# Performance work log

Hardware: AMD Instinct MI355X
Metric: run time of the kernel (lower is better)

Reference implementation:

```python
import jax, jax.numpy as jnp
import numpy as np

H = 4       # hidden size
IN = 906    # input size
B = 128
T = 512


def _lstm_dir(xp, W_hh):
    """Run a single-direction LSTM. xp: [B, T, 4H] precomputed input projection
    (x @ W_ih^T + b_ih + b_hh). Returns hidden states [B, T, H].
    Torch gate order: i, f, g, o."""
    Bb = xp.shape[0]
    h0 = jnp.zeros((Bb, H), xp.dtype)
    c0 = jnp.zeros((Bb, H), xp.dtype)

    def step(carry, g_t):
        h, c = carry
        g = g_t + h @ W_hh.T                      # [B, 4H]
        i, f, gg, o = jnp.split(g, 4, axis=-1)
        i = jax.nn.sigmoid(i)
        f = jax.nn.sigmoid(f)
        gg = jnp.tanh(gg)
        o = jax.nn.sigmoid(o)
        c = f * c + i * gg
        h = o * jnp.tanh(c)
        return (h, c), h

    xs = jnp.swapaxes(xp, 0, 1)                   # [T, B, 4H]
    _, hs = jax.lax.scan(step, (h0, c0), xs)      # hs: [T, B, H]
    return jnp.swapaxes(hs, 0, 1)                 # [B, T, H]


def setup_inputs() -> dict:
    key = jax.random.key(0)
    ks = jax.random.split(key, 12)
    s = 1.0 / np.sqrt(H)  # torch nn.LSTM init scale
    d = {
        "x": jax.random.normal(ks[0], (B, T, IN), jnp.float32),
        "W_ih_f": jax.random.normal(ks[1], (4 * H, IN), jnp.float32) * s,
        "W_hh_f": jax.random.normal(ks[2], (4 * H, H), jnp.float32) * s,
        "b_ih_f": jax.random.normal(ks[3], (4 * H,), jnp.float32) * s,
        "b_hh_f": jax.random.normal(ks[4], (4 * H,), jnp.float32) * s,
        "W_ih_b": jax.random.normal(ks[5], (4 * H, IN), jnp.float32) * s,
        "W_hh_b": jax.random.normal(ks[6], (4 * H, H), jnp.float32) * s,
        "b_ih_b": jax.random.normal(ks[7], (4 * H,), jnp.float32) * s,
        "b_hh_b": jax.random.normal(ks[8], (4 * H,), jnp.float32) * s,
        "W_out": jax.random.normal(ks[9], (2, 2 * H), jnp.float32) * s,
        "b_out": jax.random.normal(ks[10], (2,), jnp.float32) * s,
    }
    return d


def reference(x, W_ih_f, W_hh_f, b_ih_f, b_hh_f, W_ih_b, W_hh_b, b_ih_b, b_hh_b, W_out, b_out):
    # forward direction
    xp_f = x @ W_ih_f.T + (b_ih_f + b_hh_f)       # [B, T, 4H]
    out_f = _lstm_dir(xp_f, W_hh_f)               # [B, T, H]
    # backward direction: process reversed sequence, then flip back to align time
    xr = x[:, ::-1]
    xp_b = xr @ W_ih_b.T + (b_ih_b + b_hh_b)
    out_b = _lstm_dir(xp_b, W_hh_b)[:, ::-1]      # [B, T, H]
    # r_out[:, -1, :] = concat(fwd last step, bwd output at last time index)
    last = jnp.concatenate([out_f[:, -1], out_b[:, -1]], axis=-1)  # [B, 2H]
    return last @ W_out.T + b_out                 # [B, 2]
```

## Files before the change

### kernel.cpp

```cpp
#include <hip/hip_runtime.h>

#define IN 906
#define TT 512
#define NB 128

__device__ __forceinline__ float fsigm(float x) {
    float e = __builtin_amdgcn_exp2f(-1.4426950408889634f * x);
    return __builtin_amdgcn_rcpf(1.f + e);
}
__device__ __forceinline__ float ftanh(float x) {
    float e = __builtin_amdgcn_exp2f(-2.8853900817779268f * x);
    return 2.f * __builtin_amdgcn_rcpf(1.f + e) - 1.f;
}
template <int M>
__device__ __forceinline__ float quad_bcast(float v) {
    constexpr int ctrl = M | (M << 2) | (M << 4) | (M << 6);
    return __int_as_float(
        __builtin_amdgcn_mov_dpp(__float_as_int(v), ctrl, 0xf, 0xf, true));
}

__global__ __launch_bounds__(256)
void gemm_xp(const float* __restrict__ x, const float* __restrict__ W,
             const float* __restrict__ b1, const float* __restrict__ b2,
             float* __restrict__ xp)
{
    __shared__ float sx[2][32][132];
    __shared__ float sw[2][32][16];
    const int tid = threadIdx.x;
    const size_t rowbase = (size_t)blockIdx.x * 128;

    const int srow = tid >> 1;
    const int sseg = tid & 1;
    const float* __restrict__ xrow = x + (rowbase + srow) * IN + sseg * 16;
    const int wout = tid >> 4;
    const int wcc  = (tid & 15) * 2;

    const int rg = tid >> 2;
    const int og = tid & 3;
    const int r0 = rg * 2;

    float2 xr[8];
    float2 wr;
    float acc[2][4];
#pragma unroll
    for (int r = 0; r < 2; ++r)
#pragma unroll
        for (int m = 0; m < 4; ++m) acc[r][m] = 0.f;

    auto load_chunk = [&](int c) {
        const int k0 = c * 32;
        if (c < 28) {
#pragma unroll
            for (int q = 0; q < 8; ++q)
                xr[q] = *(const float2*)(xrow + k0 + q * 2);
            wr = *(const float2*)(W + wout * IN + k0 + wcc);
        } else {
#pragma unroll
            for (int q = 0; q < 8; ++q) {
                int col = k0 + sseg * 16 + q * 2;
                xr[q].x = (col     < IN) ? xrow[k0 + q * 2]     : 0.f;
                xr[q].y = (col + 1 < IN) ? xrow[k0 + q * 2 + 1] : 0.f;
            }
            int colw = k0 + wcc;
            wr.x = (colw     < IN) ? W[wout * IN + colw]     : 0.f;
            wr.y = (colw + 1 < IN) ? W[wout * IN + colw + 1] : 0.f;
        }
    };
    auto write_chunk = [&](int buf) {
#pragma unroll
        for (int q = 0; q < 8; ++q) {
            int cc = sseg * 16 + q * 2;
            sx[buf][cc][srow]     = xr[q].x;
            sx[buf][cc + 1][srow] = xr[q].y;
        }
        sw[buf][wcc][wout]     = wr.x;
        sw[buf][wcc + 1][wout] = wr.y;
    };
    auto compute = [&](int buf) {
#pragma unroll
        for (int cc = 0; cc < 32; ++cc) {
            float2 xv = *(const float2*)&sx[buf][cc][r0];
            float4 wv = *(const float4*)&sw[buf][cc][og * 4];
            acc[0][0] = fmaf(xv.x, wv.x, acc[0][0]);
            acc[0][1] = fmaf(xv.x, wv.y, acc[0][1]);
            acc[0][2] = fmaf(xv.x, wv.z, acc[0][2]);
            acc[0][3] = fmaf(xv.x, wv.w, acc[0][3]);
            acc[1][0] = fmaf(xv.y, wv.x, acc[1][0]);
            acc[1][1] = fmaf(xv.y, wv.y, acc[1][1]);
            acc[1][2] = fmaf(xv.y, wv.z, acc[1][2]);
            acc[1][3] = fmaf(xv.y, wv.w, acc[1][3]);
        }
    };

    load_chunk(0);
    write_chunk(0);
    __syncthreads();
    for (int c = 0; c < 29; ++c) {
        if (c < 28) load_chunk(c + 1);
        compute(c & 1);
        if (c < 28) write_chunk((c + 1) & 1);
        __syncthreads();
    }

#pragma unroll
    for (int rr = 0; rr < 2; ++rr) {
        const size_t row = rowbase + r0 + rr;
#pragma unroll
        for (int m = 0; m < 4; ++m) {
            int j = og * 4 + m;
            xp[row * 16 + m * 4 + og] = acc[rr][m] + b1[j] + b2[j];
        }
    }
}

__global__ __launch_bounds__(256)
void frec(const float* __restrict__ xp, const float* __restrict__ x,
          const float* __restrict__ Whh, const float* __restrict__ Wb,
          const float* __restrict__ bb1, const float* __restrict__ bb2,
          const float* __restrict__ Wout, const float* __restrict__ bout,
          float* __restrict__ out)
{
    __shared__ float bg[16][12];
    const int tid = threadIdx.x;

    float h0 = 0.f, h1 = 0.f, h2 = 0.f, h3 = 0.f;

    if (tid >= 64) {
        const int gl = tid - 64;
        const int r  = gl >> 4;
        const int bq = gl & 15;
        const int b  = blockIdx.x * 16 + bq;
        const int gr = (r < 4) ? r : r + 4;
        const float2* __restrict__ xr  = (const float2*)(x + ((size_t)b * TT + (TT - 1)) * IN);
        const float2* __restrict__ wrp = (const float2*)(Wb + gr * IN);
        float s0 = 0.f, s1 = 0.f;
        int j = 0;
        for (; j + 8 <= 453; j += 8) {
#pragma unroll
            for (int u = 0; u < 8; ++u) {
                float2 a = xr[j + u];
                float2 w = wrp[j + u];
                s0 = fmaf(a.x, w.x, s0);
                s1 = fmaf(a.y, w.y, s1);
            }
        }
        for (; j < 453; ++j) {
            float2 a = xr[j];
            float2 w = wrp[j];
            s0 = fmaf(a.x, w.x, s0);
            s1 = fmaf(a.y, w.y, s1);
        }
        bg[bq][r] = s0 + s1 + bb1[gr] + bb2[gr];
    } else {
        const int k = tid & 3;
        const int b = blockIdx.x * 16 + (tid >> 2);

        float Wi[4], Wf4[4], Wg[4], Wo[4];
#pragma unroll
        for (int m = 0; m < 4; ++m) {
            Wi[m]  = Whh[(k)      * 4 + m];
            Wf4[m] = Whh[(4 + k)  * 4 + m];
            Wg[m]  = Whh[(8 + k)  * 4 + m];
            Wo[m]  = Whh[(12 + k) * 4 + m];
        }

        const float4* __restrict__ xq = (const float4*)xp;
        const size_t base = (size_t)b * TT * 4 + k;

        float4 pf[16];
#pragma unroll
        for (int i = 0; i < 16; ++i) pf[i] = xq[base + (size_t)i * 4];

        float c = 0.f;
        for (int t = 0; t < TT; t += 16) {
#pragma unroll
            for (int u = 0; u < 16; ++u) {
                float4 cur = pf[u];
                int tn = t + 16 + u;
                int tc = (tn < TT) ? tn : (TT - 1);
                pf[u] = xq[base + (size_t)tc * 4];

                float gi = cur.x + h0 * Wi[0]  + h1 * Wi[1]  + h2 * Wi[2]  + h3 * Wi[3];
                float gf = cur.y + h0 * Wf4[0] + h1 * Wf4[1] + h2 * Wf4[2] + h3 * Wf4[3];
                float gg = cur.z + h0 * Wg[0]  + h1 * Wg[1]  + h2 * Wg[2]  + h3 * Wg[3];
                float go = cur.w + h0 * Wo[0]  + h1 * Wo[1]  + h2 * Wo[2]  + h3 * Wo[3];

                float si = fsigm(gi);
                float sf = fsigm(gf);
                float tg = ftanh(gg);
                float so = fsigm(go);

                c = sf * c + si * tg;
                float h = so * ftanh(c);

                h0 = quad_bcast<0>(h);
                h1 = quad_bcast<1>(h);
                h2 = quad_bcast<2>(h);
                h3 = quad_bcast<3>(h);
            }
        }
    }

    __syncthreads();

    if (tid < 64) {
        const int k  = tid & 3;
        const int bq = tid >> 2;
        const int b  = blockIdx.x * 16 + bq;

        float gib = bg[bq][k];
        float ggb = bg[bq][4 + k];
        float gob = bg[bq][8 + k];
        float hbk = fsigm(gob) * ftanh(fsigm(gib) * ftanh(ggb));
        float hb0 = quad_bcast<0>(hbk);
        float hb1 = quad_bcast<1>(hbk);
        float hb2 = quad_bcast<2>(hbk);
        float hb3 = quad_bcast<3>(hbk);

        float o0 = bout[0]
                 + h0  * Wout[0]  + h1  * Wout[1]  + h2  * Wout[2]  + h3  * Wout[3]
                 + hb0 * Wout[4]  + hb1 * Wout[5]  + hb2 * Wout[6]  + hb3 * Wout[7];
        float o1 = bout[1]
                 + h0  * Wout[8]  + h1  * Wout[9]  + h2  * Wout[10] + h3  * Wout[11]
                 + hb0 * Wout[12] + hb1 * Wout[13] + hb2 * Wout[14] + hb3 * Wout[15];

        if (k == 0) {
            out[b * 2 + 0] = o0;
            out[b * 2 + 1] = o1;
        }
    }
}

extern "C" void kernel_launch(void* const* d_in, const int* in_sizes, int n_in,
                              void* d_out, int out_size, void* d_ws, size_t ws_size,
                              hipStream_t stream)
{
    const float* x    = (const float*)d_in[0];
    const float* Wihf = (const float*)d_in[1];
    const float* Whhf = (const float*)d_in[2];
    const float* bihf = (const float*)d_in[3];
    const float* bhhf = (const float*)d_in[4];
    const float* Wihb = (const float*)d_in[5];
    const float* bihb = (const float*)d_in[7];
    const float* bhhb = (const float*)d_in[8];
    const float* Wout = (const float*)d_in[9];
    const float* bout = (const float*)d_in[10];

    float* xp = (float*)d_ws;

    gemm_xp<<<512, 256, 0, stream>>>(x, Wihf, bihf, bhhf, xp);
    frec<<<8, 256, 0, stream>>>(xp, x, Whhf, Wihb, bihb, bhhb, Wout, bout,
                                (float*)d_out);
}
```

Baseline: 434.9 us.

## Rewrite input-projection GEMM as split-K register accumulation with shuffle transpose-reduce

Replaces the LDS-tiled GEMM with a scheme where each wave handles 8 rows, every lane holds a k-slice, and all 8x16 outputs are accumulated in 128 registers. A recursive-halving butterfly of xor shuffles then reduces across the 64 lanes and scatters the results into xp. The shared-memory staging and per-chunk barriers go away, and x is read with coalesced float2 loads. In exchange register pressure is very high under the 2-waves-per-SIMD launch bound, the reduction adds shuffle overhead, and the grid grows to 2048 blocks.

After: 456.0 us. 1.05x slower.

```diff
diff --git a/kernel.cpp b/kernel.cpp
--- a/kernel.cpp
+++ b/kernel.cpp
@@ -19,98 +19,111 @@
         __builtin_amdgcn_mov_dpp(__float_as_int(v), ctrl, 0xf, 0xf, true));
 }
 
-__global__ __launch_bounds__(256)
+__global__ __launch_bounds__(256, 2)
 void gemm_xp(const float* __restrict__ x, const float* __restrict__ W,
              const float* __restrict__ b1, const float* __restrict__ b2,
              float* __restrict__ xp)
 {
-    __shared__ float sx[2][32][132];
-    __shared__ float sw[2][32][16];
     const int tid = threadIdx.x;
-    const size_t rowbase = (size_t)blockIdx.x * 128;
-
-    const int srow = tid >> 1;
-    const int sseg = tid & 1;
-    const float* __restrict__ xrow = x + (rowbase + srow) * IN + sseg * 16;
-    const int wout = tid >> 4;
-    const int wcc  = (tid & 15) * 2;
-
-    const int rg = tid >> 2;
-    const int og = tid & 3;
-    const int r0 = rg * 2;
-
-    float2 xr[8];
-    float2 wr;
-    float acc[2][4];
-#pragma unroll
-    for (int r = 0; r < 2; ++r)
-#pragma unroll
-        for (int m = 0; m < 4; ++m) acc[r][m] = 0.f;
-
-    auto load_chunk = [&](int c) {
-        const int k0 = c * 32;
-        if (c < 28) {
-#pragma unroll
-            for (int q = 0; q < 8; ++q)
-                xr[q] = *(const float2*)(xrow + k0 + q * 2);
-            wr = *(const float2*)(W + wout * IN + k0 + wcc);
+    const int l   = tid & 63;
+    const size_t row0 = (size_t)blockIdx.x * 32 + (size_t)(tid >> 6) * 8;
+
+    float acc[128];
+#pragma unroll
+    for (int i = 0; i < 128; ++i) acc[i] = 0.f;
+
+    const int kl = l * 2;
+
+#pragma unroll
+    for (int s = 0; s < 8; ++s) {
+        const int k = s * 128 + kl;
+        float2 wv[16];
+        float2 xv[8];
+        if (s < 7) {
+#pragma unroll
+            for (int jj = 0; jj < 16; ++jj)
+                wv[jj] = *(const float2*)(W + jj * IN + k);
+#pragma unroll
+            for (int r = 0; r < 8; ++r)
+                xv[r] = *(const float2*)(x + (row0 + r) * IN + k);
         } else {
-#pragma unroll
-            for (int q = 0; q < 8; ++q) {
-                int col = k0 + sseg * 16 + q * 2;
-                xr[q].x = (col     < IN) ? xrow[k0 + q * 2]     : 0.f;
-                xr[q].y = (col + 1 < IN) ? xrow[k0 + q * 2 + 1] : 0.f;
-            }
-            int colw = k0 + wcc;
-            wr.x = (colw     < IN) ? W[wout * IN + colw]     : 0.f;
-            wr.y = (colw + 1 < IN) ? W[wout * IN + colw + 1] : 0.f;
-        }
-    };
-    auto write_chunk = [&](int buf) {
-#pragma unroll
-        for (int q = 0; q < 8; ++q) {
-            int cc = sseg * 16 + q * 2;
-            sx[buf][cc][srow]     = xr[q].x;
-            sx[buf][cc + 1][srow] = xr[q].y;
-        }
-        sw[buf][wcc][wout]     = wr.x;
-        sw[buf][wcc + 1][wout] = wr.y;
-    };
-    auto compute = [&](int buf) {
-#pragma unroll
-        for (int cc = 0; cc < 32; ++cc) {
-            float2 xv = *(const float2*)&sx[buf][cc][r0];
-            float4 wv = *(const float4*)&sw[buf][cc][og * 4];
-            acc[0][0] = fmaf(xv.x, wv.x, acc[0][0]);
-            acc[0][1] = fmaf(xv.x, wv.y, acc[0][1]);
-            acc[0][2] = fmaf(xv.x, wv.z, acc[0][2]);
-            acc[0][3] = fmaf(xv.x, wv.w, acc[0][3]);
-            acc[1][0] = fmaf(xv.y, wv.x, acc[1][0]);
-            acc[1][1] = fmaf(xv.y, wv.y, acc[1][1]);
-            acc[1][2] = fmaf(xv.y, wv.z, acc[1][2]);
-            acc[1][3] = fmaf(xv.y, wv.w, acc[1][3]);
-        }
-    };
-
-    load_chunk(0);
-    write_chunk(0);
-    __syncthreads();
-    for (int c = 0; c < 29; ++c) {
-        if (c < 28) load_chunk(c + 1);
-        compute(c & 1);
-        if (c < 28) write_chunk((c + 1) & 1);
-        __syncthreads();
-    }
-
-#pragma unroll
-    for (int rr = 0; rr < 2; ++rr) {
-        const size_t row = rowbase + r0 + rr;
-#pragma unroll
-        for (int m = 0; m < 4; ++m) {
-            int j = og * 4 + m;
-            xp[row * 16 + m * 4 + og] = acc[rr][m] + b1[j] + b2[j];
-        }
-    }
+            const int  kc = (k < IN) ? k : 904;
+            const bool ok = (k < IN);
+#pragma unroll
+            for (int jj = 0; jj < 16; ++jj) {
+                float2 t = *(const float2*)(W + jj * IN + kc);
+                wv[jj].x = ok ? t.x : 0.f;
+                wv[jj].y = ok ? t.y : 0.f;
+            }
+#pragma unroll
+            for (int r = 0; r < 8; ++r)
+                xv[r] = *(const float2*)(x + (row0 + r) * IN + kc);
+        }
+#pragma unroll
+        for (int r = 0; r < 8; ++r)
+#pragma unroll
+            for (int jj = 0; jj < 16; ++jj) {
+                acc[r * 16 + jj] = fmaf(xv[r].x, wv[jj].x, acc[r * 16 + jj]);
+                acc[r * 16 + jj] = fmaf(xv[r].y, wv[jj].y, acc[r * 16 + jj]);
+            }
+    }
+
+    float v1[64];
+#pragma unroll
+    for (int i = 0; i < 64; ++i) {
+        float lo = acc[2 * i], hi = acc[2 * i + 1];
+        float mi = (l & 1) ? hi : lo;
+        float ot = (l & 1) ? lo : hi;
+        v1[i] = mi + __shfl_xor(ot, 1);
+    }
+    float v2[32];
+#pragma unroll
+    for (int i = 0; i < 32; ++i) {
+        float lo = v1[2 * i], hi = v1[2 * i + 1];
+        float mi = (l & 2) ? hi : lo;
+        float ot = (l & 2) ? lo : hi;
+        v2[i] = mi + __shfl_xor(ot, 2);
+    }
+    float v3[16];
+#pragma unroll
+    for (int i = 0; i < 16; ++i) {
+        float lo = v2[2 * i], hi = v2[2 * i + 1];
+        float mi = (l & 4) ? hi : lo;
+        float ot = (l & 4) ? lo : hi;
+        v3[i] = mi + __shfl_xor(ot, 4);
+    }
+    float v4[8];
+#pragma unroll
+    for (int i = 0; i < 8; ++i) {
+        float lo = v3[2 * i], hi = v3[2 * i + 1];
+        float mi = (l & 8) ? hi : lo;
+        float ot = (l & 8) ? lo : hi;
+        v4[i] = mi + __shfl_xor(ot, 8);
+    }
+    float v5[4];
+#pragma unroll
+    for (int i = 0; i < 4; ++i) {
+        float lo = v4[2 * i], hi = v4[2 * i + 1];
+        float mi = (l & 16) ? hi : lo;
+        float ot = (l & 16) ? lo : hi;
+        v5[i] = mi + __shfl_xor(ot, 16);
+    }
+    float v6[2];
+#pragma unroll
+    for (int i = 0; i < 2; ++i) {
+        float lo = v5[2 * i], hi = v5[2 * i + 1];
+        float mi = (l & 32) ? hi : lo;
+        float ot = (l & 32) ? lo : hi;
+        v6[i] = mi + __shfl_xor(ot, 32);
+    }
+
+    const int jo = l & 15;
+    const int g  = (l >> 4) & 3;
+    const int pj = (jo & 3) * 4 + (jo >> 2);
+    const float bias = b1[jo] + b2[jo];
+#pragma unroll
+    for (int p = 0; p < 2; ++p)
+        xp[(row0 + (size_t)(p * 4 + g)) * 16 + pj] = v6[p] + bias;
 }
 
 __global__ __launch_bounds__(256)
@@ -248,7 +261,7 @@
 
     float* xp = (float*)d_ws;
 
-    gemm_xp<<<512, 256, 0, stream>>>(x, Wihf, bihf, bhhf, xp);
+    gemm_xp<<<2048, 256, 0, stream>>>(x, Wihf, bihf, bhhf, xp);
     frec<<<8, 256, 0, stream>>>(xp, x, Whhf, Wihb, bihb, bhhb, Wout, bout,
                                 (float*)d_out);
 }
```

## Split GEMM K-chunk across two thread halves with 4x4 register tiles

Applied to the files above, without the earlier changes.

In the input-projection GEMM, each thread now computes a 4-row by 4-output register tile over half of each 32-wide K chunk instead of a 2x4 tile over the full chunk. The two thread halves split K and combine their partial sums through shared memory at the end. This improves the FMA-to-LDS-load ratio per thread with wider float4 row loads. It adds a final reduction pass with an extra barrier, leaves half the threads idle during the store phase, and raises per-thread register use.

Measured after the change: 433.1 us, median of 2. About the same (-0.4%).

```diff
diff --git a/kernel.cpp b/kernel.cpp
--- a/kernel.cpp
+++ b/kernel.cpp
@@ -35,15 +35,17 @@
     const int wout = tid >> 4;
     const int wcc  = (tid & 15) * 2;
 
-    const int rg = tid >> 2;
-    const int og = tid & 3;
-    const int r0 = rg * 2;
+    const int kh  = tid >> 7;
+    const int rem = tid & 127;
+    const int rg  = rem >> 2;
+    const int og  = rem & 3;
+    const int r0  = rg * 4;
 
     float2 xr[8];
     float2 wr;
-    float acc[2][4];
-#pragma unroll
-    for (int r = 0; r < 2; ++r)
+    float acc[4][4];
+#pragma unroll
+    for (int r = 0; r < 4; ++r)
 #pragma unroll
         for (int m = 0; m < 4; ++m) acc[r][m] = 0.f;
 
@@ -78,8 +80,9 @@
     };
     auto compute = [&](int buf) {
 #pragma unroll
-        for (int cc = 0; cc < 32; ++cc) {
-            float2 xv = *(const float2*)&sx[buf][cc][r0];
+        for (int cc2 = 0; cc2 < 16; ++cc2) {
+            const int cc = kh * 16 + cc2;
+            float4 xv = *(const float4*)&sx[buf][cc][r0];
             float4 wv = *(const float4*)&sw[buf][cc][og * 4];
             acc[0][0] = fmaf(xv.x, wv.x, acc[0][0]);
             acc[0][1] = fmaf(xv.x, wv.y, acc[0][1]);
@@ -89,6 +92,14 @@
             acc[1][1] = fmaf(xv.y, wv.y, acc[1][1]);
             acc[1][2] = fmaf(xv.y, wv.z, acc[1][2]);
             acc[1][3] = fmaf(xv.y, wv.w, acc[1][3]);
+            acc[2][0] = fmaf(xv.z, wv.x, acc[2][0]);
+            acc[2][1] = fmaf(xv.z, wv.y, acc[2][1]);
+            acc[2][2] = fmaf(xv.z, wv.z, acc[2][2]);
+            acc[2][3] = fmaf(xv.z, wv.w, acc[2][3]);
+            acc[3][0] = fmaf(xv.w, wv.x, acc[3][0]);
+            acc[3][1] = fmaf(xv.w, wv.y, acc[3][1]);
+            acc[3][2] = fmaf(xv.w, wv.z, acc[3][2]);
+            acc[3][3] = fmaf(xv.w, wv.w, acc[3][3]);
         }
     };
 
@@ -102,13 +113,25 @@
         __syncthreads();
     }
 
-#pragma unroll
-    for (int rr = 0; rr < 2; ++rr) {
-        const size_t row = rowbase + r0 + rr;
-#pragma unroll
-        for (int m = 0; m < 4; ++m) {
-            int j = og * 4 + m;
-            xp[row * 16 + m * 4 + og] = acc[rr][m] + b1[j] + b2[j];
+    float* red = &sx[0][0][0];
+    if (kh == 1) {
+#pragma unroll
+        for (int r = 0; r < 4; ++r)
+#pragma unroll
+            for (int m = 0; m < 4; ++m)
+                red[(r * 4 + m) * 128 + rem] = acc[r][m];
+    }
+    __syncthreads();
+    if (kh == 0) {
+#pragma unroll
+        for (int r = 0; r < 4; ++r) {
+            const size_t row = rowbase + r0 + r;
+#pragma unroll
+            for (int m = 0; m < 4; ++m) {
+                const int j = og * 4 + m;
+                float v = acc[r][m] + red[(r * 4 + m) * 128 + rem];
+                xp[row * 16 + m * 4 + og] = v + b1[j] + b2[j];
+            }
         }
     }
 }
```

## Restructure input-projection GEMM with split-K, 4x4 register tiles and swizzled LDS

Applied to the files above, without the earlier changes.

The x·W_ih projection kernel now uses 64-row tiles with 64-wide K chunks and 128-bit vector global loads. Each wave handles a quarter of every K chunk, and a 4x4 register tile reads swizzled LDS rows. The partial sums are combined through shared memory at the end, and twice as many blocks are launched. The aim is to raise memory-load throughput and occupancy on this bandwidth-bound GEMM, at the cost of an extra reduction pass and possibly misaligned 16-byte loads, since IN=906 leaves rows not 16-byte aligned.

Measured after the change: 435.4 us. About the same (+0.1%).

```diff
diff --git a/kernel.cpp b/kernel.cpp
--- a/kernel.cpp
+++ b/kernel.cpp
@@ -3,6 +3,14 @@
 #define IN 906
 #define TT 512
 #define NB 128
+
+typedef float fv4 __attribute__((ext_vector_type(4)));
+
+__device__ __forceinline__ fv4 ldg4(const float* p) {
+    fv4 v;
+    __builtin_memcpy(&v, p, 16);
+    return v;
+}
 
 __device__ __forceinline__ float fsigm(float x) {
     float e = __builtin_amdgcn_exp2f(-1.4426950408889634f * x);
@@ -24,91 +32,115 @@
              const float* __restrict__ b1, const float* __restrict__ b2,
              float* __restrict__ xp)
 {
-    __shared__ float sx[2][32][132];
-    __shared__ float sw[2][32][16];
+    __shared__ float sx[2][64][64];
+    __shared__ float sw[2][16][64];
     const int tid = threadIdx.x;
-    const size_t rowbase = (size_t)blockIdx.x * 128;
-
-    const int srow = tid >> 1;
-    const int sseg = tid & 1;
-    const float* __restrict__ xrow = x + (rowbase + srow) * IN + sseg * 16;
-    const int wout = tid >> 4;
-    const int wcc  = (tid & 15) * 2;
-
-    const int rg = tid >> 2;
+    const size_t rowbase = (size_t)blockIdx.x * 64;
+
+    const int srow = tid >> 2;
+    const int sseg = tid & 3;
+    const int sxsw = (srow >> 2) & 7;
+    const int wrow = tid >> 4;
+    const int wseg = tid & 15;
+    const int wssw = (wrow >> 2) & 3;
+
+    const int kq = tid >> 6;
+    const int rg = (tid >> 2) & 15;
     const int og = tid & 3;
-    const int r0 = rg * 2;
-
-    float2 xr[8];
-    float2 wr;
-    float acc[2][4];
-#pragma unroll
-    for (int r = 0; r < 2; ++r)
-#pragma unroll
-        for (int m = 0; m < 4; ++m) acc[r][m] = 0.f;
+
+    float acc[4][4] = {};
+    fv4 xr[4];
+    fv4 wr;
+
+    const float* __restrict__ xrow = x + (rowbase + srow) * IN;
+    const float* __restrict__ wrp  = W + wrow * IN;
 
     auto load_chunk = [&](int c) {
-        const int k0 = c * 32;
-        if (c < 28) {
-#pragma unroll
-            for (int q = 0; q < 8; ++q)
-                xr[q] = *(const float2*)(xrow + k0 + q * 2);
-            wr = *(const float2*)(W + wout * IN + k0 + wcc);
+        const int k0 = c * 64;
+        if (c < 14) {
+#pragma unroll
+            for (int q = 0; q < 4; ++q)
+                xr[q] = ldg4(xrow + k0 + (q * 4 + sseg) * 4);
+            wr = ldg4(wrp + k0 + wseg * 4);
         } else {
 #pragma unroll
-            for (int q = 0; q < 8; ++q) {
-                int col = k0 + sseg * 16 + q * 2;
-                xr[q].x = (col     < IN) ? xrow[k0 + q * 2]     : 0.f;
-                xr[q].y = (col + 1 < IN) ? xrow[k0 + q * 2 + 1] : 0.f;
-            }
-            int colw = k0 + wcc;
-            wr.x = (colw     < IN) ? W[wout * IN + colw]     : 0.f;
-            wr.y = (colw + 1 < IN) ? W[wout * IN + colw + 1] : 0.f;
+            for (int q = 0; q < 4; ++q) {
+                const int col0 = k0 + (q * 4 + sseg) * 4;
+#pragma unroll
+                for (int e = 0; e < 4; ++e)
+                    xr[q][e] = (col0 + e < IN) ? xrow[col0 + e] : 0.f;
+            }
+            const int colw0 = k0 + wseg * 4;
+#pragma unroll
+            for (int e = 0; e < 4; ++e)
+                wr[e] = (colw0 + e < IN) ? wrp[colw0 + e] : 0.f;
         }
     };
     auto write_chunk = [&](int buf) {
 #pragma unroll
-        for (int q = 0; q < 8; ++q) {
-            int cc = sseg * 16 + q * 2;
-            sx[buf][cc][srow]     = xr[q].x;
-            sx[buf][cc + 1][srow] = xr[q].y;
-        }
-        sw[buf][wcc][wout]     = wr.x;
-        sw[buf][wcc + 1][wout] = wr.y;
+        for (int q = 0; q < 4; ++q) {
+            const int cg = q * 4 + sseg;
+            *(fv4*)&sx[buf][srow][(cg ^ sxsw) * 4] = xr[q];
+        }
+        *(fv4*)&sw[buf][wrow][(wseg ^ wssw) * 4] = wr;
     };
     auto compute = [&](int buf) {
 #pragma unroll
-        for (int cc = 0; cc < 32; ++cc) {
-            float2 xv = *(const float2*)&sx[buf][cc][r0];
-            float4 wv = *(const float4*)&sw[buf][cc][og * 4];
-            acc[0][0] = fmaf(xv.x, wv.x, acc[0][0]);
-            acc[0][1] = fmaf(xv.x, wv.y, acc[0][1]);
-            acc[0][2] = fmaf(xv.x, wv.z, acc[0][2]);
-            acc[0][3] = fmaf(xv.x, wv.w, acc[0][3]);
-            acc[1][0] = fmaf(xv.y, wv.x, acc[1][0]);
-            acc[1][1] = fmaf(xv.y, wv.y, acc[1][1]);
-            acc[1][2] = fmaf(xv.y, wv.z, acc[1][2]);
-            acc[1][3] = fmaf(xv.y, wv.w, acc[1][3]);
+        for (int cg2 = 0; cg2 < 4; ++cg2) {
+            const int cg = kq * 4 + cg2;
+            const int xs = (cg ^ (rg & 7)) * 4;
+            const int ws = (cg ^ og) * 4;
+            fv4 xv[4], wv[4];
+#pragma unroll
+            for (int ri = 0; ri < 4; ++ri)
+                xv[ri] = *(const fv4*)&sx[buf][rg * 4 + ri][xs];
+#pragma unroll
+            for (int jj = 0; jj < 4; ++jj)
+                wv[jj] = *(const fv4*)&sw[buf][og * 4 + jj][ws];
+#pragma unroll
+            for (int ri = 0; ri < 4; ++ri)
+#pragma unroll
+                for (int jj = 0; jj < 4; ++jj)
+#pragma unroll
+                    for (int e = 0; e < 4; ++e)
+                        acc[ri][jj] = fmaf(xv[ri][e], wv[jj][e], acc[ri][jj]);
         }
     };
 
     load_chunk(0);
     write_chunk(0);
     __syncthreads();
-    for (int c = 0; c < 29; ++c) {
-        if (c < 28) load_chunk(c + 1);
+    for (int c = 0; c < 15; ++c) {
+        if (c < 14) load_chunk(c + 1);
         compute(c & 1);
-        if (c < 28) write_chunk((c + 1) & 1);
+        if (c < 14) write_chunk((c + 1) & 1);
         __syncthreads();
     }
 
-#pragma unroll
-    for (int rr = 0; rr < 2; ++rr) {
-        const size_t row = rowbase + r0 + rr;
-#pragma unroll
-        for (int m = 0; m < 4; ++m) {
-            int j = og * 4 + m;
-            xp[row * 16 + m * 4 + og] = acc[rr][m] + b1[j] + b2[j];
+    float* red = &sx[0][0][0];
+    const int idx = tid & 63;
+    if (kq != 0) {
+        float* rp = red + ((kq - 1) * 64 + idx) * 17;
+#pragma unroll
+        for (int ri = 0; ri < 4; ++ri)
+#pragma unroll
+            for (int jj = 0; jj < 4; ++jj)
+                rp[ri * 4 + jj] = acc[ri][jj];
+    }
+    __syncthreads();
+    if (kq == 0) {
+#pragma unroll
+        for (int ri = 0; ri < 4; ++ri) {
+            const size_t row = rowbase + rg * 4 + ri;
+#pragma unroll
+            for (int jj = 0; jj < 4; ++jj) {
+                float t = acc[ri][jj]
+                        + red[(0 * 64 + idx) * 17 + ri * 4 + jj]
+                        + red[(1 * 64 + idx) * 17 + ri * 4 + jj]
+                        + red[(2 * 64 + idx) * 17 + ri * 4 + jj];
+                const int j = og * 4 + jj;
+                xp[row * 16 + jj * 4 + og] = t + b1[j] + b2[j];
+            }
         }
     }
 }
@@ -248,7 +280,7 @@
 
     float* xp = (float*)d_ws;
 
-    gemm_xp<<<512, 256, 0, stream>>>(x, Wihf, bihf, bhhf, xp);
+    gemm_xp<<<1024, 256, 0, stream>>>(x, Wihf, bihf, bhhf, xp);
     frec<<<8, 256, 0, stream>>>(xp, x, Whhf, Wihb, bihb, bhhb, Wout, bout,
                                 (float*)d_out);
 }
```
